# Kernel tuning notes

Measured on AMD Instinct MI355X. Metric: run time of the kernel, lower is better.

## Reference

```python
import jax, jax.numpy as jnp
import numpy as np

DIM = 512
HEADS = 8
HEAD_DIM = DIM // HEADS
HIDDEN = 4 * DIM
EPS = 1e-5


def _ln(x, g, b):
    mu = jnp.mean(x, axis=-1, keepdims=True)
    var = jnp.mean((x - mu) ** 2, axis=-1, keepdims=True)
    return (x - mu) * jax.lax.rsqrt(var + EPS) * g + b


def setup_inputs() -> dict:
    key = jax.random.key(0)
    ks = jax.random.split(key, 12)
    s = lambda fan: 1.0 / np.sqrt(fan)
    return {
        "x": jax.random.normal(ks[0], (2, 4096, DIM), jnp.float32),
        "ln1_g": jnp.ones((DIM,), jnp.float32),
        "ln1_b": jnp.zeros((DIM,), jnp.float32),
        "ln2_g": jnp.ones((DIM,), jnp.float32),
        "ln2_b": jnp.zeros((DIM,), jnp.float32),
        "qkv_w": jax.random.normal(ks[1], (3 * DIM, DIM), jnp.float32) * s(DIM),
        "qkv_b": jnp.zeros((3 * DIM,), jnp.float32),
        "proj_w": jax.random.normal(ks[2], (DIM, DIM), jnp.float32) * s(DIM),
        "proj_b": jnp.zeros((DIM,), jnp.float32),
        "fc1_w": jax.random.normal(ks[3], (HIDDEN, DIM), jnp.float32) * s(DIM),
        "fc1_b": jnp.zeros((HIDDEN,), jnp.float32),
        "fc2_w": jax.random.normal(ks[4], (DIM, HIDDEN), jnp.float32) * s(HIDDEN),
        "fc2_b": jnp.zeros((DIM,), jnp.float32),
    }


def reference(x, ln1_g, ln1_b, ln2_g, ln2_b, qkv_w, qkv_b, proj_w, proj_b,
              fc1_w, fc1_b, fc2_w, fc2_b):
    B, N, C = x.shape
    # --- attention (pre-norm) ---
    h = _ln(x, ln1_g, ln1_b)
    qkv = h @ qkv_w.T + qkv_b                      # [B,N,3C]
    qkv = qkv.reshape(B, N, 3, HEADS, HEAD_DIM)
    q, k, v = (jnp.moveaxis(qkv, 2, 0)[i].transpose(0, 2, 1, 3) for i in range(3))  # [B,H,N,D]
    scale = HEAD_DIM ** -0.5
    attn = jax.nn.softmax(jnp.einsum('bhnd,bhmd->bhnm', q, k) * scale, axis=-1)
    out = jnp.einsum('bhnm,bhmd->bhnd', attn, v)   # [B,H,N,D]
    out = out.transpose(0, 2, 1, 3).reshape(B, N, C)
    x = x + out @ proj_w.T + proj_b
    # --- MLP (pre-norm) ---
    h = _ln(x, ln2_g, ln2_b)
    h = jax.nn.gelu(h @ fc1_w.T + fc1_b, approximate=False)
    return x + h @ fc2_w.T + fc2_b
```

## Files before the change

### kernel.cpp

```cpp
#include <hip/hip_runtime.h>
#include <hip/hip_bf16.h>
#include <hip/hip_fp16.h>
#include <string.h>

using bf16 = __hip_bfloat16;
typedef __attribute__((ext_vector_type(8))) short short8;
typedef __attribute__((ext_vector_type(8))) _Float16 half8;
typedef __attribute__((ext_vector_type(4))) float f32x4;
typedef __attribute__((ext_vector_type(16))) float f32x16;

#define GAS __attribute__((address_space(1)))
#define LAS __attribute__((address_space(3)))

__device__ __forceinline__ void gld_lds16(const void* g, void* l) {
  __builtin_amdgcn_global_load_lds((const GAS void*)g, (LAS void*)l, 16, 0, 0);
}

__device__ __forceinline__ unsigned short f2bfu(float f) {
  bf16 h = __float2bfloat16(f);
  return *reinterpret_cast<unsigned short*>(&h);
}

__device__ __forceinline__ unsigned pack_bf16x2(float lo, float hi) {
  __hip_bfloat162 v = __float22bfloat162_rn(make_float2(lo, hi));
  unsigned u;
  __builtin_memcpy(&u, &v, 4);
  return u;
}

__device__ __forceinline__ unsigned pack_f16x2(float lo, float hi) {
  __half2 v = __float22half2_rn(make_float2(lo, hi));
  unsigned u;
  __builtin_memcpy(&u, &v, 4);
  return u;
}

__global__ __launch_bounds__(256) void cvt_all(const float* __restrict__ w0, bf16* __restrict__ o0,
                                               const float* __restrict__ w1, bf16* __restrict__ o1,
                                               const float* __restrict__ w2, bf16* __restrict__ o2,
                                               const float* __restrict__ w3, bf16* __restrict__ o3) {
  int i = blockIdx.x * 256 + threadIdx.x;
  const float* src; bf16* dst; int off;
  if (i < 196608)      { src = w0; dst = o0; off = i; }
  else if (i < 262144) { src = w1; dst = o1; off = i - 196608; }
  else if (i < 524288) { src = w2; dst = o2; off = i - 262144; }
  else                 { src = w3; dst = o3; off = i - 524288; }
  float4 v = reinterpret_cast<const float4*>(src)[off];
  ushort4 o;
  o.x = f2bfu(v.x); o.y = f2bfu(v.y); o.z = f2bfu(v.z); o.w = f2bfu(v.w);
  reinterpret_cast<ushort4*>(dst)[off] = o;
}

__global__ __launch_bounds__(256) void ln_kernel(const float* __restrict__ x,
                                                 const float* __restrict__ g,
                                                 const float* __restrict__ b,
                                                 bf16* __restrict__ out) {
  const int row = blockIdx.x * 4 + (threadIdx.x >> 6);
  const int lane = threadIdx.x & 63;
  const float4* xr = reinterpret_cast<const float4*>(x + (size_t)row * 512);
  float4 v0 = xr[lane], v1 = xr[64 + lane];
  float s  = v0.x + v0.y + v0.z + v0.w + v1.x + v1.y + v1.z + v1.w;
  float s2 = v0.x*v0.x + v0.y*v0.y + v0.z*v0.z + v0.w*v0.w
           + v1.x*v1.x + v1.y*v1.y + v1.z*v1.z + v1.w*v1.w;
  #pragma unroll
  for (int d = 1; d < 64; d <<= 1) { s += __shfl_xor(s, d); s2 += __shfl_xor(s2, d); }
  const float mu = s * (1.0f / 512.0f);
  const float var = s2 * (1.0f / 512.0f) - mu * mu;
  const float rstd = rsqrtf(var + 1e-5f);
  const float4* g4 = reinterpret_cast<const float4*>(g);
  const float4* b4 = reinterpret_cast<const float4*>(b);
  float4 ga = g4[lane], gb = g4[64 + lane], ba = b4[lane], bb = b4[64 + lane];
  ushort4 o0, o1;
  o0.x = f2bfu((v0.x - mu) * rstd * ga.x + ba.x);
  o0.y = f2bfu((v0.y - mu) * rstd * ga.y + ba.y);
  o0.z = f2bfu((v0.z - mu) * rstd * ga.z + ba.z);
  o0.w = f2bfu((v0.w - mu) * rstd * ga.w + ba.w);
  o1.x = f2bfu((v1.x - mu) * rstd * gb.x + bb.x);
  o1.y = f2bfu((v1.y - mu) * rstd * gb.y + bb.y);
  o1.z = f2bfu((v1.z - mu) * rstd * gb.z + bb.z);
  o1.w = f2bfu((v1.w - mu) * rstd * gb.w + bb.w);
  ushort4* orow = reinterpret_cast<ushort4*>(out + (size_t)row * 512);
  orow[lane] = o0;
  orow[64 + lane] = o1;
}

template <int EPI>
__global__ __launch_bounds__(256) void gemm_bt(const bf16* __restrict__ A,
                                               const bf16* __restrict__ B,
                                               const float* __restrict__ bias,
                                               const float* __restrict__ resid,
                                               void* __restrict__ Cv,
                                               int M, int N, int K) {
  __shared__ bf16 As[128 * 32];
  __shared__ bf16 Bs[128 * 32];
  const int tid = threadIdx.x;
  const int lane = tid & 63, wid = tid >> 6;
  const int lr = lane & 15, lg = lane >> 4;
  const int row0 = blockIdx.x * 128, col0 = blockIdx.y * 128;
  const int wr = (wid >> 1) * 64, wc = (wid & 1) * 64;
  f32x4 acc[4][4] = {};
  const int r1 = tid >> 2,          c1 = (tid & 3) * 8;
  const int r2 = (256 + tid) >> 2,  c2 = ((256 + tid) & 3) * 8;
  for (int kt = 0; kt < K; kt += 32) {
    __syncthreads();
    gld_lds16(A + (size_t)(row0 + r1) * K + kt + c1, As + tid * 8);
    gld_lds16(A + (size_t)(row0 + r2) * K + kt + c2, As + (256 + tid) * 8);
    gld_lds16(B + (size_t)(col0 + r1) * K + kt + c1, Bs + tid * 8);
    gld_lds16(B + (size_t)(col0 + r2) * K + kt + c2, Bs + (256 + tid) * 8);
    __syncthreads();
    short8 af[4], bfr[4];
    #pragma unroll
    for (int mi = 0; mi < 4; ++mi)
      af[mi] = *reinterpret_cast<const short8*>(&As[(wr + mi * 16 + lr) * 32 + lg * 8]);
    #pragma unroll
    for (int nj = 0; nj < 4; ++nj)
      bfr[nj] = *reinterpret_cast<const short8*>(&Bs[(wc + nj * 16 + lr) * 32 + lg * 8]);
    #pragma unroll
    for (int mi = 0; mi < 4; ++mi)
      #pragma unroll
      for (int nj = 0; nj < 4; ++nj)
        acc[mi][nj] = __builtin_amdgcn_mfma_f32_16x16x32_bf16(af[mi], bfr[nj], acc[mi][nj], 0, 0, 0);
  }
  #pragma unroll
  for (int mi = 0; mi < 4; ++mi) {
    #pragma unroll
    for (int nj = 0; nj < 4; ++nj) {
      const int col = col0 + wc + nj * 16 + lr;
      const float bv = bias ? bias[col] : 0.0f;
      #pragma unroll
      for (int rg = 0; rg < 4; ++rg) {
        const int row = row0 + wr + mi * 16 + lg * 4 + rg;
        float v = acc[mi][nj][rg] + bv;
        if constexpr (EPI == 1) v = 0.5f * v * (1.0f + erff(v * 0.70710678118654752f));
        if constexpr (EPI == 2) {
          reinterpret_cast<float*>(Cv)[(size_t)row * N + col] = v + resid[(size_t)row * N + col];
        } else if constexpr (EPI == 3) {
          reinterpret_cast<__half*>(Cv)[(size_t)row * N + col] = __float2half(v);
        } else {
          reinterpret_cast<bf16*>(Cv)[(size_t)row * N + col] = __float2bfloat16(v);
        }
      }
    }
  }
}

template <int EPI>
__global__ __launch_bounds__(256) void gemm_bt64(const bf16* __restrict__ A,
                                                 const bf16* __restrict__ B,
                                                 const float* __restrict__ bias,
                                                 const float* __restrict__ resid,
                                                 void* __restrict__ Cv,
                                                 int M, int N, int K) {
  __shared__ bf16 As[64 * 64];
  __shared__ bf16 Bs[64 * 64];
  const int tid = threadIdx.x;
  const int lane = tid & 63, wid = tid >> 6;
  const int lr = lane & 15, lg = lane >> 4;
  const int row0 = blockIdx.x * 64, col0 = blockIdx.y * 64;
  const int wr = (wid >> 1) * 32, wc = (wid & 1) * 32;
  f32x4 acc[2][2] = {};
  const int xsw = (lr & 7) << 4;
  const int fb0 = lr * 128 + ((lg * 16) ^ xsw);
  const int fb1 = lr * 128 + ((64 + lg * 16) ^ xsw);
  const int ph0 = tid * 16, ph1 = (256 + tid) * 16;
  const int r0 = ph0 >> 7, r1 = ph1 >> 7;
  const int lb0 = ph0 ^ ((r0 & 7) << 4), lb1 = ph1 ^ ((r1 & 7) << 4);
  const char* Ab0 = (const char*)A + (size_t)(row0 + r0) * K * 2 + (lb0 & 127);
  const char* Ab1 = (const char*)A + (size_t)(row0 + r1) * K * 2 + (lb1 & 127);
  const char* Bb0 = (const char*)B + (size_t)(col0 + r0) * K * 2 + (lb0 & 127);
  const char* Bb1 = (const char*)B + (size_t)(col0 + r1) * K * 2 + (lb1 & 127);
  for (int kt = 0; kt < K; kt += 64) {
    __syncthreads();
    gld_lds16(Ab0 + kt * 2, (char*)As + ph0);
    gld_lds16(Ab1 + kt * 2, (char*)As + ph1);
    gld_lds16(Bb0 + kt * 2, (char*)Bs + ph0);
    gld_lds16(Bb1 + kt * 2, (char*)Bs + ph1);
    __syncthreads();
    short8 af0[2], af1[2], bf0[2], bf1[2];
    #pragma unroll
    for (int mi = 0; mi < 2; ++mi) {
      af0[mi] = *reinterpret_cast<const short8*>((const char*)As + (wr + mi * 16) * 128 + fb0);
      af1[mi] = *reinterpret_cast<const short8*>((const char*)As + (wr + mi * 16) * 128 + fb1);
    }
    #pragma unroll
    for (int nj = 0; nj < 2; ++nj) {
      bf0[nj] = *reinterpret_cast<const short8*>((const char*)Bs + (wc + nj * 16) * 128 + fb0);
      bf1[nj] = *reinterpret_cast<const short8*>((const char*)Bs + (wc + nj * 16) * 128 + fb1);
    }
    #pragma unroll
    for (int mi = 0; mi < 2; ++mi)
      #pragma unroll
      for (int nj = 0; nj < 2; ++nj) {
        acc[mi][nj] = __builtin_amdgcn_mfma_f32_16x16x32_bf16(af0[mi], bf0[nj], acc[mi][nj], 0, 0, 0);
        acc[mi][nj] = __builtin_amdgcn_mfma_f32_16x16x32_bf16(af1[mi], bf1[nj], acc[mi][nj], 0, 0, 0);
      }
  }
  #pragma unroll
  for (int mi = 0; mi < 2; ++mi) {
    #pragma unroll
    for (int nj = 0; nj < 2; ++nj) {
      const int col = col0 + wc + nj * 16 + lr;
      const float bv = bias ? bias[col] : 0.0f;
      #pragma unroll
      for (int rg = 0; rg < 4; ++rg) {
        const int row = row0 + wr + mi * 16 + lg * 4 + rg;
        float v = acc[mi][nj][rg] + bv;
        if constexpr (EPI == 1) v = 0.5f * v * (1.0f + erff(v * 0.70710678118654752f));
        if constexpr (EPI == 2) {
          reinterpret_cast<float*>(Cv)[(size_t)row * N + col] = v + resid[(size_t)row * N + col];
        } else {
          reinterpret_cast<bf16*>(Cv)[(size_t)row * N + col] = __float2bfloat16(v);
        }
      }
    }
  }
}

__global__ __launch_bounds__(256) void reshape_qkv(const __half* __restrict__ C,
                                                   __half* __restrict__ q,
                                                   __half* __restrict__ KF,
                                                   __half* __restrict__ VF) {
  const int nt = blockIdx.x;
  const int bh = blockIdx.y;
  const int b = bh >> 3, h = bh & 7;
  __shared__ alignas(16) __half vs[64][72];
  const int tid = threadIdx.x;
  const float qs = 0.125f * 1.44269504088896340736f;
  #pragma unroll
  for (int i = 0; i < 16; ++i) {
    const int idx = i * 256 + tid;
    const int rr = idx >> 6, c = idx & 63;
    const size_t crow = ((size_t)b * 4096 + nt * 64 + rr) * 1536;
    const size_t onb = ((size_t)bh * 4096 + nt * 64 + rr) * 64 + c;
    q[onb] = __float2half(__half2float(C[crow + h * 64 + c]) * qs);
    vs[c][rr] = C[crow + 1024 + h * 64 + c];
  }
  #pragma unroll
  for (int i = 0; i < 2; ++i) {
    const int s = i * 256 + tid;
    const int half_ = s >> 8, dc = (s >> 6) & 3, l = s & 63;
    const int l31 = l & 31, hi2 = l >> 5;
    const __half* src = C + ((size_t)b * 4096 + nt * 64 + half_ * 32 + l31) * 1536
                          + 512 + h * 64 + dc * 16 + hi2 * 8;
    __half* dst = KF + ((size_t)bh * 128 + nt * 2 + half_) * 2048 + dc * 512 + (size_t)l * 8;
    *reinterpret_cast<short8*>(dst) = *reinterpret_cast<const short8*>(src);
  }
  __syncthreads();
  #pragma unroll
  for (int i = 0; i < 2; ++i) {
    const int s = i * 256 + tid;
    const int half_ = (s >> 8) & 1, db = (s >> 7) & 1, c = (s >> 6) & 1, l = s & 63;
    const int d = db * 32 + (l & 31);
    const int n0 = half_ * 32 + c * 16 + ((l >> 5) << 2);
    const short4 lo = *reinterpret_cast<const short4*>(&vs[d][n0]);
    const short4 hi = *reinterpret_cast<const short4*>(&vs[d][n0 + 8]);
    short8 v;
    v[0] = lo.x; v[1] = lo.y; v[2] = lo.z; v[3] = lo.w;
    v[4] = hi.x; v[5] = hi.y; v[6] = hi.z; v[7] = hi.w;
    __half* dst = VF + ((size_t)bh * 128 + nt * 2 + half_) * 2048 + (db * 2 + c) * 512 + (size_t)l * 8;
    *reinterpret_cast<short8*>(dst) = v;
  }
}

__global__ __launch_bounds__(256, 2) void attn_kernel(const __half* __restrict__ Q,
                                                      const __half* __restrict__ KF,
                                                      const __half* __restrict__ VF,
                                                      bf16* __restrict__ Out) {
  const int qt = blockIdx.x;
  const int bh = blockIdx.y;
  const int b = bh >> 3, h = bh & 7;
  __shared__ alignas(16) char smem[17408];
  const int tid = threadIdx.x, w = tid >> 6, lane = tid & 63;
  const int qg = w >> 1, kvh = w & 1;
  const int l31 = lane & 31, hi = lane >> 5;

  const __half* qbase = Q + ((size_t)bh * 4096 + qt * 128 + qg * 64 + l31) * 64 + hi * 8;
  half8 qf0[4], qf1[4];
  #pragma unroll
  for (int dc = 0; dc < 4; ++dc) {
    qf0[dc] = *reinterpret_cast<const half8*>(qbase + dc * 16);
    qf1[dc] = *reinterpret_cast<const half8*>(qbase + 2048 + dc * 16);
  }

  const char* kfp = (const char*)KF + (size_t)bh * 524288 + (size_t)kvh * 262144 + lane * 16;
  const char* vfp = (const char*)VF + (size_t)bh * 524288 + (size_t)kvh * 262144 + lane * 16;

  f32x16 O00 = {}, O01 = {};
  f32x16 O10 = {}, O11 = {};
  float m0 = -1e30f, l0 = 0.0f, m1 = -1e30f, l1 = 0.0f;

  for (int t = 0; t < 64; ++t) {
    const half8 va00 = *reinterpret_cast<const half8*>(vfp);
    const half8 va01 = *reinterpret_cast<const half8*>(vfp + 1024);
    const half8 va10 = *reinterpret_cast<const half8*>(vfp + 2048);
    const half8 va11 = *reinterpret_cast<const half8*>(vfp + 3072);
    vfp += 4096;
    const half8 kf0 = *reinterpret_cast<const half8*>(kfp);
    const half8 kf1 = *reinterpret_cast<const half8*>(kfp + 1024);
    const half8 kf2 = *reinterpret_cast<const half8*>(kfp + 2048);
    const half8 kf3 = *reinterpret_cast<const half8*>(kfp + 3072);
    kfp += 4096;
    f32x16 S0 = {}, S1 = {};
    __builtin_amdgcn_s_setprio(1);
    S0 = __builtin_amdgcn_mfma_f32_32x32x16_f16(kf0, qf0[0], S0, 0, 0, 0);
    S1 = __builtin_amdgcn_mfma_f32_32x32x16_f16(kf0, qf1[0], S1, 0, 0, 0);
    S0 = __builtin_amdgcn_mfma_f32_32x32x16_f16(kf1, qf0[1], S0, 0, 0, 0);
    S1 = __builtin_amdgcn_mfma_f32_32x32x16_f16(kf1, qf1[1], S1, 0, 0, 0);
    S0 = __builtin_amdgcn_mfma_f32_32x32x16_f16(kf2, qf0[2], S0, 0, 0, 0);
    S1 = __builtin_amdgcn_mfma_f32_32x32x16_f16(kf2, qf1[2], S1, 0, 0, 0);
    S0 = __builtin_amdgcn_mfma_f32_32x32x16_f16(kf3, qf0[3], S0, 0, 0, 0);
    S1 = __builtin_amdgcn_mfma_f32_32x32x16_f16(kf3, qf1[3], S1, 0, 0, 0);
    __builtin_amdgcn_s_setprio(0);
    union U8 { unsigned u[4]; half8 h8; } p00, p01, p10, p11;
    {
      float a0 = fmaxf(fmaxf(S0[0], S0[1]), fmaxf(S0[2], S0[3]));
      float a1 = fmaxf(fmaxf(S0[4], S0[5]), fmaxf(S0[6], S0[7]));
      float a2 = fmaxf(fmaxf(S0[8], S0[9]), fmaxf(S0[10], S0[11]));
      float a3 = fmaxf(fmaxf(S0[12], S0[13]), fmaxf(S0[14], S0[15]));
      float rmax = fmaxf(fmaxf(a0, a1), fmaxf(a2, a3));
      rmax = fmaxf(rmax, __shfl_xor(rmax, 32));
      if (!__all(rmax <= m0 + 8.0f)) {
        const float mnew = fmaxf(m0, rmax);
        const float fsc = __builtin_amdgcn_exp2f(m0 - mnew);
        l0 *= fsc;
        #pragma unroll
        for (int i = 0; i < 16; ++i) { O00[i] *= fsc; O01[i] *= fsc; }
        m0 = mnew;
      }
      #pragma unroll
      for (int i = 0; i < 16; ++i) S0[i] = __builtin_amdgcn_exp2f(S0[i] - m0);
      float s0 = (S0[0] + S0[1]) + (S0[2] + S0[3]);
      float s1 = (S0[4] + S0[5]) + (S0[6] + S0[7]);
      float s2 = (S0[8] + S0[9]) + (S0[10] + S0[11]);
      float s3 = (S0[12] + S0[13]) + (S0[14] + S0[15]);
      float rsum = (s0 + s1) + (s2 + s3);
      rsum += __shfl_xor(rsum, 32);
      l0 += rsum;
      p00.u[0] = pack_f16x2(S0[0], S0[1]);   p00.u[1] = pack_f16x2(S0[2], S0[3]);
      p00.u[2] = pack_f16x2(S0[4], S0[5]);   p00.u[3] = pack_f16x2(S0[6], S0[7]);
      p01.u[0] = pack_f16x2(S0[8], S0[9]);   p01.u[1] = pack_f16x2(S0[10], S0[11]);
      p01.u[2] = pack_f16x2(S0[12], S0[13]); p01.u[3] = pack_f16x2(S0[14], S0[15]);
    }
    {
      float a0 = fmaxf(fmaxf(S1[0], S1[1]), fmaxf(S1[2], S1[3]));
      float a1 = fmaxf(fmaxf(S1[4], S1[5]), fmaxf(S1[6], S1[7]));
      float a2 = fmaxf(fmaxf(S1[8], S1[9]), fmaxf(S1[10], S1[11]));
      float a3 = fmaxf(fmaxf(S1[12], S1[13]), fmaxf(S1[14], S1[15]));
      float rmax = fmaxf(fmaxf(a0, a1), fmaxf(a2, a3));
      rmax = fmaxf(rmax, __shfl_xor(rmax, 32));
      if (!__all(rmax <= m1 + 8.0f)) {
        const float mnew = fmaxf(m1, rmax);
        const float fsc = __builtin_amdgcn_exp2f(m1 - mnew);
        l1 *= fsc;
        #pragma unroll
        for (int i = 0; i < 16; ++i) { O10[i] *= fsc; O11[i] *= fsc; }
        m1 = mnew;
      }
      #pragma unroll
      for (int i = 0; i < 16; ++i) S1[i] = __builtin_amdgcn_exp2f(S1[i] - m1);
      float s0 = (S1[0] + S1[1]) + (S1[2] + S1[3]);
      float s1 = (S1[4] + S1[5]) + (S1[6] + S1[7]);
      float s2 = (S1[8] + S1[9]) + (S1[10] + S1[11]);
      float s3 = (S1[12] + S1[13]) + (S1[14] + S1[15]);
      float rsum = (s0 + s1) + (s2 + s3);
      rsum += __shfl_xor(rsum, 32);
      l1 += rsum;
      p10.u[0] = pack_f16x2(S1[0], S1[1]);   p10.u[1] = pack_f16x2(S1[2], S1[3]);
      p10.u[2] = pack_f16x2(S1[4], S1[5]);   p10.u[3] = pack_f16x2(S1[6], S1[7]);
      p11.u[0] = pack_f16x2(S1[8], S1[9]);   p11.u[1] = pack_f16x2(S1[10], S1[11]);
      p11.u[2] = pack_f16x2(S1[12], S1[13]); p11.u[3] = pack_f16x2(S1[14], S1[15]);
    }
    __builtin_amdgcn_s_setprio(1);
    O00 = __builtin_amdgcn_mfma_f32_32x32x16_f16(va00, p00.h8, O00, 0, 0, 0);
    O10 = __builtin_amdgcn_mfma_f32_32x32x16_f16(va00, p10.h8, O10, 0, 0, 0);
    O00 = __builtin_amdgcn_mfma_f32_32x32x16_f16(va01, p01.h8, O00, 0, 0, 0);
    O10 = __builtin_amdgcn_mfma_f32_32x32x16_f16(va01, p11.h8, O10, 0, 0, 0);
    O01 = __builtin_amdgcn_mfma_f32_32x32x16_f16(va10, p00.h8, O01, 0, 0, 0);
    O11 = __builtin_amdgcn_mfma_f32_32x32x16_f16(va10, p10.h8, O11, 0, 0, 0);
    O01 = __builtin_amdgcn_mfma_f32_32x32x16_f16(va11, p01.h8, O01, 0, 0, 0);
    O11 = __builtin_amdgcn_mfma_f32_32x32x16_f16(va11, p11.h8, O11, 0, 0, 0);
    __builtin_amdgcn_s_setprio(0);
  }

  float* area = reinterpret_cast<float*>(smem) + qg * 2176;
  #pragma unroll
  for (int qs = 0; qs < 2; ++qs) {
    const f32x16& Pd0 = qs ? O10 : O00;
    const f32x16& Pd1 = qs ? O11 : O01;
    const float mw = qs ? m1 : m0;
    const float lw = qs ? l1 : l0;
    __syncthreads();
    if (kvh) {
      #pragma unroll
      for (int r = 0; r < 16; ++r) {
        area[r * 64 + lane] = Pd0[r];
        area[(16 + r) * 64 + lane] = Pd1[r];
      }
      area[2048 + lane] = mw;
      area[2112 + lane] = lw;
    }
    __syncthreads();
    if (!kvh) {
      const float mB = area[2048 + lane], lB = area[2112 + lane];
      const float mx = fmaxf(mw, mB);
      const float fa = __builtin_amdgcn_exp2f(mw - mx);
      const float fb = __builtin_amdgcn_exp2f(mB - mx);
      const float inv = 1.0f / (lw * fa + lB * fb);
      const int qrow2 = qt * 128 + qg * 64 + qs * 32 + l31;
      bf16* ob = Out + ((size_t)b * 4096 + qrow2) * 512 + h * 64 + hi * 4;
      #pragma unroll
      for (int db = 0; db < 2; ++db) {
        #pragma unroll
        for (int rq = 0; rq < 4; ++rq) {
          const int r = rq * 4;
          float v0 = ((db ? Pd1[r + 0] : Pd0[r + 0]) * fa + area[(db * 16 + r + 0) * 64 + lane] * fb) * inv;
          float v1 = ((db ? Pd1[r + 1] : Pd0[r + 1]) * fa + area[(db * 16 + r + 1) * 64 + lane] * fb) * inv;
          float v2 = ((db ? Pd1[r + 2] : Pd0[r + 2]) * fa + area[(db * 16 + r + 2) * 64 + lane] * fb) * inv;
          float v3 = ((db ? Pd1[r + 3] : Pd0[r + 3]) * fa + area[(db * 16 + r + 3) * 64 + lane] * fb) * inv;
          uint2 st;
          st.x = pack_bf16x2(v0, v1);
          st.y = pack_bf16x2(v2, v3);
          *reinterpret_cast<uint2*>(ob + db * 32 + rq * 8) = st;
        }
      }
    }
  }
}

extern "C" void kernel_launch(void* const* d_in, const int* in_sizes, int n_in,
                              void* d_out, int out_size, void* d_ws, size_t ws_size,
                              hipStream_t stream) {
  const float* x      = (const float*)d_in[0];
  const float* ln1_g  = (const float*)d_in[1];
  const float* ln1_b  = (const float*)d_in[2];
  const float* ln2_g  = (const float*)d_in[3];
  const float* ln2_b  = (const float*)d_in[4];
  const float* qkv_w  = (const float*)d_in[5];
  const float* qkv_b  = (const float*)d_in[6];
  const float* proj_w = (const float*)d_in[7];
  const float* proj_b = (const float*)d_in[8];
  const float* fc1_w  = (const float*)d_in[9];
  const float* fc1_b  = (const float*)d_in[10];
  const float* fc2_w  = (const float*)d_in[11];
  const float* fc2_b  = (const float*)d_in[12];

  char* ws = (char*)d_ws;
  constexpr size_t o_qkvw = 0;
  constexpr size_t o_projw = 1572864;
  constexpr size_t o_fc1w  = 2097152;
  constexpr size_t o_fc2w  = 4194304;
  constexpr size_t o_h     = 6291456;
  constexpr size_t o_qkvC  = 14680064;
  constexpr size_t o_q     = 39845888;
  constexpr size_t o_k     = 48234496;
  constexpr size_t o_vt    = 56623104;
  constexpr size_t o_attn  = 65011712;
  constexpr size_t o_x2    = 73400320;
  constexpr size_t o_fc1o  = o_qkvC;
  constexpr size_t needed  = 90177536;
  if (ws_size < needed) return;

  bf16* qkvw_bf = (bf16*)(ws + o_qkvw);
  bf16* projw_bf = (bf16*)(ws + o_projw);
  bf16* fc1w_bf = (bf16*)(ws + o_fc1w);
  bf16* fc2w_bf = (bf16*)(ws + o_fc2w);
  bf16* h     = (bf16*)(ws + o_h);
  __half* qkvC = (__half*)(ws + o_qkvC);
  __half* q    = (__half*)(ws + o_q);
  __half* kf   = (__half*)(ws + o_k);
  __half* vf   = (__half*)(ws + o_vt);
  bf16* attn  = (bf16*)(ws + o_attn);
  float* x2   = (float*)(ws + o_x2);
  bf16* fc1o  = (bf16*)(ws + o_fc1o);
  float* out  = (float*)d_out;

  cvt_all<<<3072, 256, 0, stream>>>(qkv_w, qkvw_bf, proj_w, projw_bf, fc1_w, fc1w_bf, fc2_w, fc2w_bf);

  ln_kernel<<<2048, 256, 0, stream>>>(x, ln1_g, ln1_b, h);
  gemm_bt<3><<<dim3(64, 12), 256, 0, stream>>>(h, qkvw_bf, qkv_b, nullptr, qkvC, 8192, 1536, 512);
  reshape_qkv<<<dim3(64, 16), 256, 0, stream>>>(qkvC, q, kf, vf);
  attn_kernel<<<dim3(32, 16), 256, 0, stream>>>(q, kf, vf, attn);
  gemm_bt64<2><<<dim3(128, 8), 256, 0, stream>>>(attn, projw_bf, proj_b, x, x2, 8192, 512, 512);
  ln_kernel<<<2048, 256, 0, stream>>>(x2, ln2_g, ln2_b, h);
  gemm_bt<1><<<dim3(64, 16), 256, 0, stream>>>(h, fc1w_bf, fc1_b, nullptr, fc1o, 8192, 2048, 512);
  gemm_bt64<2><<<dim3(128, 8), 256, 0, stream>>>(fc1o, fc2w_bf, fc2_b, x2, out, 8192, 512, 2048);
}
```

Baseline: 237.6 us.

## Split attention KV range across four waves per 64-query tile

The attention block now covers 64 queries instead of 128, with all four waves sharing the same queries and each taking a quarter of the KV sequence. The grid doubles to 1024 blocks and launch bounds rise to 4 blocks per SM for more parallelism and occupancy. Partial softmax states are merged serially through shared memory into wave 0, which adds sync rounds and extra LDS traffic. Each block reads the full K/V once for only 64 queries, so total K/V global traffic doubles, and the higher launch bound may pressure registers.

Measured after the change: 393.3 us. 1.66x slower.

```diff
diff --git a/kernel.cpp b/kernel.cpp
--- a/kernel.cpp
+++ b/kernel.cpp
@@ -262,7 +262,7 @@
   }
 }
 
-__global__ __launch_bounds__(256, 2) void attn_kernel(const __half* __restrict__ Q,
+__global__ __launch_bounds__(256, 4) void attn_kernel(const __half* __restrict__ Q,
                                                       const __half* __restrict__ KF,
                                                       const __half* __restrict__ VF,
                                                       bf16* __restrict__ Out) {
@@ -271,10 +271,9 @@
   const int b = bh >> 3, h = bh & 7;
   __shared__ alignas(16) char smem[17408];
   const int tid = threadIdx.x, w = tid >> 6, lane = tid & 63;
-  const int qg = w >> 1, kvh = w & 1;
   const int l31 = lane & 31, hi = lane >> 5;
 
-  const __half* qbase = Q + ((size_t)bh * 4096 + qt * 128 + qg * 64 + l31) * 64 + hi * 8;
+  const __half* qbase = Q + ((size_t)bh * 4096 + qt * 64 + l31) * 64 + hi * 8;
   half8 qf0[4], qf1[4];
   #pragma unroll
   for (int dc = 0; dc < 4; ++dc) {
@@ -282,14 +281,14 @@
     qf1[dc] = *reinterpret_cast<const half8*>(qbase + 2048 + dc * 16);
   }
 
-  const char* kfp = (const char*)KF + (size_t)bh * 524288 + (size_t)kvh * 262144 + lane * 16;
-  const char* vfp = (const char*)VF + (size_t)bh * 524288 + (size_t)kvh * 262144 + lane * 16;
+  const char* kfp = (const char*)KF + (size_t)bh * 524288 + (size_t)w * 131072 + lane * 16;
+  const char* vfp = (const char*)VF + (size_t)bh * 524288 + (size_t)w * 131072 + lane * 16;
 
   f32x16 O00 = {}, O01 = {};
   f32x16 O10 = {}, O11 = {};
   float m0 = -1e30f, l0 = 0.0f, m1 = -1e30f, l1 = 0.0f;
 
-  for (int t = 0; t < 64; ++t) {
+  for (int t = 0; t < 32; ++t) {
     const half8 va00 = *reinterpret_cast<const half8*>(vfp);
     const half8 va01 = *reinterpret_cast<const half8*>(vfp + 1024);
     const half8 va10 = *reinterpret_cast<const half8*>(vfp + 2048);
@@ -382,44 +381,69 @@
     __builtin_amdgcn_s_setprio(0);
   }
 
-  float* area = reinterpret_cast<float*>(smem) + qg * 2176;
-  #pragma unroll
-  for (int qs = 0; qs < 2; ++qs) {
-    const f32x16& Pd0 = qs ? O10 : O00;
-    const f32x16& Pd1 = qs ? O11 : O01;
-    const float mw = qs ? m1 : m0;
-    const float lw = qs ? l1 : l0;
+  float* area0 = reinterpret_cast<float*>(smem);
+  float* area1 = reinterpret_cast<float*>(smem) + 2176;
+  for (int r = 1; r < 4; ++r) {
     __syncthreads();
-    if (kvh) {
-      #pragma unroll
-      for (int r = 0; r < 16; ++r) {
-        area[r * 64 + lane] = Pd0[r];
-        area[(16 + r) * 64 + lane] = Pd1[r];
-      }
-      area[2048 + lane] = mw;
-      area[2112 + lane] = lw;
+    if (w == r) {
+      #pragma unroll
+      for (int i = 0; i < 16; ++i) {
+        area0[i * 64 + lane] = O00[i];
+        area0[(16 + i) * 64 + lane] = O01[i];
+        area1[i * 64 + lane] = O10[i];
+        area1[(16 + i) * 64 + lane] = O11[i];
+      }
+      area0[2048 + lane] = m0;  area0[2112 + lane] = l0;
+      area1[2048 + lane] = m1;  area1[2112 + lane] = l1;
     }
     __syncthreads();
-    if (!kvh) {
-      const float mB = area[2048 + lane], lB = area[2112 + lane];
-      const float mx = fmaxf(mw, mB);
-      const float fa = __builtin_amdgcn_exp2f(mw - mx);
-      const float fb = __builtin_amdgcn_exp2f(mB - mx);
-      const float inv = 1.0f / (lw * fa + lB * fb);
-      const int qrow2 = qt * 128 + qg * 64 + qs * 32 + l31;
+    if (w == 0) {
+      {
+        const float mB = area0[2048 + lane], lB = area0[2112 + lane];
+        const float mx = fmaxf(m0, mB);
+        const float fa = __builtin_amdgcn_exp2f(m0 - mx);
+        const float fb = __builtin_amdgcn_exp2f(mB - mx);
+        #pragma unroll
+        for (int i = 0; i < 16; ++i) {
+          O00[i] = O00[i] * fa + area0[i * 64 + lane] * fb;
+          O01[i] = O01[i] * fa + area0[(16 + i) * 64 + lane] * fb;
+        }
+        l0 = l0 * fa + lB * fb;
+        m0 = mx;
+      }
+      {
+        const float mB = area1[2048 + lane], lB = area1[2112 + lane];
+        const float mx = fmaxf(m1, mB);
+        const float fa = __builtin_amdgcn_exp2f(m1 - mx);
+        const float fb = __builtin_amdgcn_exp2f(mB - mx);
+        #pragma unroll
+        for (int i = 0; i < 16; ++i) {
+          O10[i] = O10[i] * fa + area1[i * 64 + lane] * fb;
+          O11[i] = O11[i] * fa + area1[(16 + i) * 64 + lane] * fb;
+        }
+        l1 = l1 * fa + lB * fb;
+        m1 = mx;
+      }
+    }
+  }
+  if (w == 0) {
+    #pragma unroll
+    for (int qs = 0; qs < 2; ++qs) {
+      const f32x16& Pd0 = qs ? O10 : O00;
+      const f32x16& Pd1 = qs ? O11 : O01;
+      const float inv = 1.0f / (qs ? l1 : l0);
+      const int qrow2 = qt * 64 + qs * 32 + l31;
       bf16* ob = Out + ((size_t)b * 4096 + qrow2) * 512 + h * 64 + hi * 4;
       #pragma unroll
       for (int db = 0; db < 2; ++db) {
         #pragma unroll
         for (int rq = 0; rq < 4; ++rq) {
           const int r = rq * 4;
-          float v0 = ((db ? Pd1[r + 0] : Pd0[r + 0]) * fa + area[(db * 16 + r + 0) * 64 + lane] * fb) * inv;
-          float v1 = ((db ? Pd1[r + 1] : Pd0[r + 1]) * fa + area[(db * 16 + r + 1) * 64 + lane] * fb) * inv;
-          float v2 = ((db ? Pd1[r + 2] : Pd0[r + 2]) * fa + area[(db * 16 + r + 2) * 64 + lane] * fb) * inv;
-          float v3 = ((db ? Pd1[r + 3] : Pd0[r + 3]) * fa + area[(db * 16 + r + 3) * 64 + lane] * fb) * inv;
           uint2 st;
-          st.x = pack_bf16x2(v0, v1);
-          st.y = pack_bf16x2(v2, v3);
+          st.x = pack_bf16x2((db ? Pd1[r + 0] : Pd0[r + 0]) * inv,
+                             (db ? Pd1[r + 1] : Pd0[r + 1]) * inv);
+          st.y = pack_bf16x2((db ? Pd1[r + 2] : Pd0[r + 2]) * inv,
+                             (db ? Pd1[r + 3] : Pd0[r + 3]) * inv);
           *reinterpret_cast<uint2*>(ob + db * 32 + rq * 8) = st;
         }
       }
@@ -479,7 +503,7 @@
   ln_kernel<<<2048, 256, 0, stream>>>(x, ln1_g, ln1_b, h);
   gemm_bt<3><<<dim3(64, 12), 256, 0, stream>>>(h, qkvw_bf, qkv_b, nullptr, qkvC, 8192, 1536, 512);
   reshape_qkv<<<dim3(64, 16), 256, 0, stream>>>(qkvC, q, kf, vf);
-  attn_kernel<<<dim3(32, 16), 256, 0, stream>>>(q, kf, vf, attn);
+  attn_kernel<<<dim3(64, 16), 256, 0, stream>>>(q, kf, vf, attn);
   gemm_bt64<2><<<dim3(128, 8), 256, 0, stream>>>(attn, projw_bf, proj_b, x, x2, 8192, 512, 512);
   ln_kernel<<<2048, 256, 0, stream>>>(x2, ln2_g, ln2_b, h);
   gemm_bt<1><<<dim3(64, 16), 256, 0, stream>>>(h, fc1w_bf, fc1_b, nullptr, fc1o, 8192, 2048, 512);
```
